# Performance work log

Measured on AMD Instinct MI355X. Metric: run time of the kernel, lower is better.

Reference implementation:

```python
import jax, jax.numpy as jnp
import numpy as np

V, E, HL, HH, T_STEPS, N_STEPS = 32000, 768, 1024, 768, 5, 3
B, S = 8, 256
EPS = 1e-5


def _ln(x, g, b):
    m = jnp.mean(x, axis=-1, keepdims=True)
    v = jnp.var(x, axis=-1, keepdims=True)
    return (x - m) * jax.lax.rsqrt(v + EPS) * g + b


def _gru(x, h, Wi, bi, Wh, bh, lni_g, lni_b, lnh_g, lnh_b):
    # Wi: [3, in_dim, H]; gates stacked in order (r, z, n)
    xi = jnp.einsum('bd,kdh->kbh', x, Wi) + bi[:, None, :]
    hi = jnp.einsum('bh,khg->kbg', h, Wh) + bh[:, None, :]
    xi = _ln(xi, lni_g[:, None, :], lni_b[:, None, :])
    hi = _ln(hi, lnh_g[:, None, :], lnh_b[:, None, :])
    r = jax.nn.sigmoid(xi[0] + hi[0])
    z = jax.nn.sigmoid(xi[1] + hi[1])
    n = jnp.tanh(xi[2] + r * hi[2])
    return (1.0 - z) * n + z * h


def setup_inputs() -> dict:
    key = jax.random.key(0)
    ks = jax.random.split(key, 12)
    lin = E + HH  # low-level cell input dim (x concat h_h)

    def xavier(k, shape, fan_in, fan_out):
        lim = float(np.sqrt(6.0 / (fan_in + fan_out)))
        return jax.random.uniform(k, shape, jnp.float32, -lim, lim)

    inp = {
        'input_ids': jax.random.randint(ks[0], (B, S), 0, V),
        'emb': xavier(ks[1], (V, E), V, E),
        'ln_emb_g': jnp.ones((E,), jnp.float32),
        'ln_emb_b': jnp.zeros((E,), jnp.float32),
        'low_Wi': xavier(ks[2], (3, lin, HL), lin, HL),
        'low_bi': jnp.zeros((3, HL), jnp.float32),
        'low_Wh': xavier(ks[3], (3, HL, HL), HL, HL),
        'low_bh': jnp.zeros((3, HL), jnp.float32),
        'low_lni_g': jnp.ones((3, HL), jnp.float32),
        'low_lni_b': jnp.zeros((3, HL), jnp.float32),
        'low_lnh_g': jnp.ones((3, HL), jnp.float32),
        'low_lnh_b': jnp.zeros((3, HL), jnp.float32),
        'high_Wi': xavier(ks[4], (3, HL, HH), HL, HH),
        'high_bi': jnp.zeros((3, HH), jnp.float32),
        'high_Wh': xavier(ks[5], (3, HH, HH), HH, HH),
        'high_bh': jnp.zeros((3, HH), jnp.float32),
        'high_lni_g': jnp.ones((3, HH), jnp.float32),
        'high_lni_b': jnp.zeros((3, HH), jnp.float32),
        'high_lnh_g': jnp.ones((3, HH), jnp.float32),
        'high_lnh_b': jnp.zeros((3, HH), jnp.float32),
        'Wout': xavier(ks[6], (HH, V), HH, V),
        'bout': jnp.zeros((V,), jnp.float32),
    }
    return inp


def reference(input_ids, emb, ln_emb_g, ln_emb_b,
              low_Wi, low_bi, low_Wh, low_bh,
              low_lni_g, low_lni_b, low_lnh_g, low_lnh_b,
              high_Wi, high_bi, high_Wh, high_bh,
              high_lni_g, high_lni_b, high_lnh_g, high_lnh_b,
              Wout, bout):
    b = input_ids.shape[0]
    h_l0 = jnp.zeros((b, HL), jnp.float32)
    h_h0 = jnp.zeros((b, HH), jnp.float32)

    def step(carry, ids_t):
        h_l, h_h = carry
        x = _ln(emb[ids_t], ln_emb_g, ln_emb_b)  # [B, E]
        for _ in range(N_STEPS):
            for _ in range(T_STEPS):
                h_l = _gru(jnp.concatenate([x, h_h], axis=-1), h_l,
                           low_Wi, low_bi, low_Wh, low_bh,
                           low_lni_g, low_lni_b, low_lnh_g, low_lnh_b)
            h_h = _gru(h_l, h_h,
                       high_Wi, high_bi, high_Wh, high_bh,
                       high_lni_g, high_lni_b, high_lnh_g, high_lnh_b)
        logits_t = h_h @ Wout + bout  # [B, V]
        return (h_l, h_h), logits_t

    _, logits = jax.lax.scan(step, (h_l0, h_h0), input_ids.T)  # [S, B, V]
    return jnp.transpose(logits, (1, 0, 2))  # [B, S, V]
```

## Files before the change

kernel.cpp:

```cpp
#include <hip/hip_runtime.h>
#include <hip/hip_bf16.h>


#define NWG 128
#define NTH 256
#define EPSV 1e-5f

typedef __attribute__((ext_vector_type(4))) float f32x4;
typedef __attribute__((ext_vector_type(8))) short short8;
typedef unsigned long long u64;

struct PArgs {
  const int* ids; const float* emb; const float* lng; const float* lnb;
  const float* lWi; const float* lbi; const float* lWh; const float* lbh;
  const float* llig; const float* llib; const float* llhg; const float* llhb;
  const float* hWi; const float* hbi; const float* hWh; const float* hbh;
  const float* hlig; const float* hlib; const float* hlhg; const float* hlhb;
  int* arr; int* rel; u64* statsG; u64* sredG; float* hlR; float* hhR;
  __hip_bfloat16* hist; float* WiT; float* hWiT; float* hWhT;
};

__device__ __forceinline__ float sigm(float x) { return 1.f / (1.f + __expf(-x)); }
__device__ __forceinline__ float tanh_f(float x) {
  x = fminf(15.f, fmaxf(-15.f, x));
  float e = __expf(2.f * x);
  return (e - 1.f) / (e + 1.f);
}
__device__ __forceinline__ void ast(float* p, float v) {
  __hip_atomic_store(p, v, __ATOMIC_RELAXED, __HIP_MEMORY_SCOPE_AGENT);
}
__device__ __forceinline__ int aldi(const int* p) {
  return __hip_atomic_load(p, __ATOMIC_RELAXED, __HIP_MEMORY_SCOPE_AGENT);
}
__device__ __forceinline__ u64 aldu(const u64* p) {
  return __hip_atomic_load(p, __ATOMIC_RELAXED, __HIP_MEMORY_SCOPE_AGENT);
}
__device__ __forceinline__ void astu(u64* p, u64 v) {
  __hip_atomic_store(p, v, __ATOMIC_RELAXED, __HIP_MEMORY_SCOPE_AGENT);
}
__device__ __forceinline__ void asti(int* p, int v) {
  __hip_atomic_store(p, v, __ATOMIC_RELAXED, __HIP_MEMORY_SCOPE_AGENT);
}
__device__ __forceinline__ void ald4x2(const float* p0, const float* p1,
                                       float4& a, float4& b) {
  asm volatile(
      "global_load_dwordx4 %0, %2, off sc1\n\t"
      "global_load_dwordx4 %1, %3, off sc1\n\t"
      "s_waitcnt vmcnt(0)"
      : "=&v"(a), "=&v"(b)
      : "v"(p0), "v"(p1)
      : "memory");
}
__device__ __forceinline__ void ald4x4(const float* p0, const float* p1,
                                       const float* p2, const float* p3,
                                       float4& a, float4& b, float4& c, float4& d) {
  asm volatile(
      "global_load_dwordx4 %0, %4, off sc1\n\t"
      "global_load_dwordx4 %1, %5, off sc1\n\t"
      "global_load_dwordx4 %2, %6, off sc1\n\t"
      "global_load_dwordx4 %3, %7, off sc1\n\t"
      "s_waitcnt vmcnt(0)"
      : "=&v"(a), "=&v"(b), "=&v"(c), "=&v"(d)
      : "v"(p0), "v"(p1), "v"(p2), "v"(p3)
      : "memory");
}
__device__ __forceinline__ void ald4x8(const float* p0, const float* p1,
                                       const float* p2, const float* p3,
                                       const float* p4, const float* p5,
                                       const float* p6, const float* p7,
                                       float4& a, float4& b, float4& c, float4& d,
                                       float4& e, float4& f, float4& g, float4& h) {
  asm volatile(
      "global_load_dwordx4 %0, %8, off sc1\n\t"
      "global_load_dwordx4 %1, %9, off sc1\n\t"
      "global_load_dwordx4 %2, %10, off sc1\n\t"
      "global_load_dwordx4 %3, %11, off sc1\n\t"
      "global_load_dwordx4 %4, %12, off sc1\n\t"
      "global_load_dwordx4 %5, %13, off sc1\n\t"
      "global_load_dwordx4 %6, %14, off sc1\n\t"
      "global_load_dwordx4 %7, %15, off sc1\n\t"
      "s_waitcnt vmcnt(0)"
      : "=&v"(a), "=&v"(b), "=&v"(c), "=&v"(d),
        "=&v"(e), "=&v"(f), "=&v"(g), "=&v"(h)
      : "v"(p0), "v"(p1), "v"(p2), "v"(p3),
        "v"(p4), "v"(p5), "v"(p6), "v"(p7)
      : "memory");
}

__global__ void __launch_bounds__(NTH) hrm_recur(PArgs P) {
  const int tid = threadIdx.x;

  if (blockIdx.x == NWG) {
    __shared__ float mbuf[192][4];
    __shared__ int mok;
    auto mevent = [&](int e, int lo, int n, float invD, int par) -> bool {
      if (tid < 64) {
        const u64* ap = (const u64*)P.arr + tid;
        int lim = 1 << 22, good = 1;
        for (;;) {
          u64 v = aldu(ap);
          int a0 = (int)(unsigned)(v & 0xffffffffull);
          int a1 = (int)(unsigned)(v >> 32);
          if (__all(a0 >= e && a1 >= e)) break;
          if (--lim == 0) { good = 0; break; }
          __builtin_amdgcn_s_sleep(1);
        }
        if (tid == 0) mok = good;
      }
      __syncthreads();
      bool good = (mok != 0);
      if (good && n > 0) {
        const int rpn = n >> 1;
        const int Q = (n == 48) ? 8 : 16;
        const int wpq = 128 / Q;
        if (tid < rpn * Q) {
          int rp = (lo >> 1) + tid / Q, q = tid % Q;
          const float* b0 = (const float*)(P.statsG + (size_t)par * 128 * 48);
          float4 s; s.x = 0.f; s.y = 0.f; s.z = 0.f; s.w = 0.f;
          #pragma unroll
          for (int blk = 0; blk < 2; ++blk) {
            if (blk == 1 && wpq == 8) break;
            int w0 = q * wpq + blk * 8;
            float4 t0,t1,t2,t3,t4,t5,t6,t7;
            ald4x8(b0 + ((size_t)(w0+0)*48 + rp*2)*2, b0 + ((size_t)(w0+1)*48 + rp*2)*2,
                   b0 + ((size_t)(w0+2)*48 + rp*2)*2, b0 + ((size_t)(w0+3)*48 + rp*2)*2,
                   b0 + ((size_t)(w0+4)*48 + rp*2)*2, b0 + ((size_t)(w0+5)*48 + rp*2)*2,
                   b0 + ((size_t)(w0+6)*48 + rp*2)*2, b0 + ((size_t)(w0+7)*48 + rp*2)*2,
                   t0,t1,t2,t3,t4,t5,t6,t7);
            s.x += t0.x+t1.x+t2.x+t3.x+t4.x+t5.x+t6.x+t7.x;
            s.y += t0.y+t1.y+t2.y+t3.y+t4.y+t5.y+t6.y+t7.y;
            s.z += t0.z+t1.z+t2.z+t3.z+t4.z+t5.z+t6.z+t7.z;
            s.w += t0.w+t1.w+t2.w+t3.w+t4.w+t5.w+t6.w+t7.w;
          }
          mbuf[tid][0] = s.x; mbuf[tid][1] = s.y; mbuf[tid][2] = s.z; mbuf[tid][3] = s.w;
        }
        __syncthreads();
        if (tid < n) {
          int rpl = tid >> 1, comp = tid & 1;
          const int Q2 = (n == 48) ? 8 : 16;
          float s1 = 0.f, s2 = 0.f;
          for (int q = 0; q < Q2; ++q) {
            s1 += mbuf[rpl * Q2 + q][comp * 2 + 0];
            s2 += mbuf[rpl * Q2 + q][comp * 2 + 1];
          }
          float m = s1 * invD;
          float rs = rsqrtf(s2 * invD - m * m + EPSV);
          union { u64 u; float f[2]; } c; c.f[0] = m; c.f[1] = rs;
          astu(P.sredG + (size_t)par * 48 + lo + tid, c.u);
        }
        asm volatile("s_waitcnt vmcnt(0)" ::: "memory");
        __syncthreads();
      }
      int pub = good ? e : (1 << 30);
      if (tid < 8) asti(P.rel + tid * 16, pub);
      return good;
    };

    if (!mevent(1, 0, 0, 0.f, 0)) return;
    int rr = 0;
    #pragma unroll 1
    for (int t = 0; t < 256; ++t) {
      #pragma unroll 1
      for (int nn = 0; nn < 3; ++nn) {
        ++rr;
        if (!mevent(2*rr, 0, 48, 1.f/1024.f, rr & 1)) return;
        if (!mevent(2*rr + 1, 0, 0, 0.f, 0)) return;
        #pragma unroll 1
        for (int it = 1; it < 5; ++it) {
          ++rr;
          if (!mevent(2*rr, 24, 24, 1.f/1024.f, rr & 1)) return;
          if (!mevent(2*rr + 1, 0, 0, 0.f, 0)) return;
        }
        ++rr;
        if (!mevent(2*rr, 0, 48, 1.f/768.f, rr & 1)) return;
        if (!mevent(2*rr + 1, 0, 0, 0.f, 0)) return;
      }
    }
    return;
  }

  __shared__ float WhS[24 * 1024];
  __shared__ float Bb[8 * 1024];
  __shared__ float XW[24 * 8];
  __shared__ float xiNs[24 * 8];
  __shared__ float stg[2][24 * 8];
  __shared__ float sred[96];
  __shared__ float xm[8], xrs[8];
  __shared__ int idsh[8];
  __shared__ int okf;

  const int wg = blockIdx.x;
  const int ks = tid & 31, cg = tid >> 5;
  const int lj8 = wg * 8, lj6 = wg * 6;
  const int rep = wg & 3;

  auto arrive = [&](int e) {
    asm volatile("s_waitcnt vmcnt(0)" ::: "memory");
    __syncthreads();
    if (tid == 0) asti(P.arr + wg, e);
  };
  auto wwait = [&](int e) -> bool {
    if (tid == 0) {
      const int* rp = P.rel + (wg & 7) * 16;
      int lim = 1 << 22, v = 0;
      do {
        v = aldi(rp);
        if (v >= e) break;
        __builtin_amdgcn_s_sleep(1);
      } while (--lim);
      okf = (lim != 0 && v < (1 << 29)) ? 1 : 0;
    }
    __syncthreads();
    return okf != 0;
  };

  auto stage_hl = [&]() {
    const float* base = P.hlR + (size_t)rep * 8192 + tid * 4;
    float4 t0,t1,t2,t3,t4,t5,t6,t7;
    ald4x8(base + 0*1024, base + 1*1024, base + 2*1024, base + 3*1024,
           base + 4*1024, base + 5*1024, base + 6*1024, base + 7*1024,
           t0,t1,t2,t3,t4,t5,t6,t7);
    *(float4*)&Bb[0*1024 + tid*4] = t0; *(float4*)&Bb[1*1024 + tid*4] = t1;
    *(float4*)&Bb[2*1024 + tid*4] = t2; *(float4*)&Bb[3*1024 + tid*4] = t3;
    *(float4*)&Bb[4*1024 + tid*4] = t4; *(float4*)&Bb[5*1024 + tid*4] = t5;
    *(float4*)&Bb[6*1024 + tid*4] = t6; *(float4*)&Bb[7*1024 + tid*4] = t7;
  };
  auto stage_hh = [&]() {
    const float* base = P.hhR + (size_t)rep * 6144;
    int bi[6], ki[6];
    #pragma unroll
    for (int i = 0; i < 6; ++i) {
      int c = i * 256 + tid; int b = c / 192; int k = (c - b * 192) * 4;
      bi[i] = b; ki[i] = k;
    }
    float4 t0,t1,t2,t3,t4,t5;
    ald4x4(base + bi[0]*768 + ki[0], base + bi[1]*768 + ki[1],
           base + bi[2]*768 + ki[2], base + bi[3]*768 + ki[3], t0,t1,t2,t3);
    ald4x2(base + bi[4]*768 + ki[4], base + bi[5]*768 + ki[5], t4,t5);
    *(float4*)&Bb[bi[0]*1024 + ki[0]] = t0; *(float4*)&Bb[bi[1]*1024 + ki[1]] = t1;
    *(float4*)&Bb[bi[2]*1024 + ki[2]] = t2; *(float4*)&Bb[bi[3]*1024 + ki[3]] = t3;
    *(float4*)&Bb[bi[4]*1024 + ki[4]] = t4; *(float4*)&Bb[bi[5]*1024 + ki[5]] = t5;
  };

  auto gemm_lowh = [&](float (&acc)[3][8]) {
    const int c0 = cg * 3;
    const float* w0p = &WhS[(c0 + 0) * 1024];
    const float* w1p = &WhS[(c0 + 1) * 1024];
    const float* w2p = &WhS[(c0 + 2) * 1024];
    #pragma unroll
    for (int i = 0; i < 8; ++i) {
      int k = i * 128 + ks * 4;
      float4 w0 = *(const float4*)&w0p[k];
      float4 w1 = *(const float4*)&w1p[k];
      float4 w2 = *(const float4*)&w2p[k];
      #pragma unroll
      for (int b = 0; b < 8; ++b) {
        float4 h = *(const float4*)&Bb[b * 1024 + k];
        acc[0][b] += w0.x*h.x + w0.y*h.y + w0.z*h.z + w0.w*h.w;
        acc[1][b] += w1.x*h.x + w1.y*h.y + w1.z*h.z + w1.w*h.w;
        acc[2][b] += w2.x*h.x + w2.y*h.y + w2.z*h.z + w2.w*h.w;
      }
    }
  };
  auto gemm_xih = [&](float (&acc)[3][8]) {
    const float* wp[3];
    #pragma unroll
    for (int cc = 0; cc < 3; ++cc) {
      int c = cg * 3 + cc; int g = c >> 3, jj = c & 7;
      wp[cc] = P.WiT + ((size_t)g * 1024 + lj8 + jj) * 1536 + 768;
    }
    #pragma unroll
    for (int i = 0; i < 6; ++i) {
      int k = i * 128 + ks * 4;
      float4 w0 = *(const float4*)&wp[0][k];
      float4 w1 = *(const float4*)&wp[1][k];
      float4 w2 = *(const float4*)&wp[2][k];
      #pragma unroll
      for (int b = 0; b < 8; ++b) {
        float4 h = *(const float4*)&Bb[b * 1024 + k];
        acc[0][b] += w0.x*h.x + w0.y*h.y + w0.z*h.z + w0.w*h.w;
        acc[1][b] += w1.x*h.x + w1.y*h.y + w1.z*h.z + w1.w*h.w;
        acc[2][b] += w2.x*h.x + w2.y*h.y + w2.z*h.z + w2.w*h.w;
      }
    }
  };
  auto gemm_hxi = [&](float (&acc)[3][8]) {
    if (cg >= 6) return;
    const float* wp[3];
    #pragma unroll
    for (int cc = 0; cc < 3; ++cc) {
      int c = cg * 3 + cc; int g = c / 6, jj = c % 6;
      wp[cc] = P.hWiT + ((size_t)g * 768 + lj6 + jj) * 1024;
    }
    #pragma unroll
    for (int i = 0; i < 8; ++i) {
      int k = i * 128 + ks * 4;
      float4 w0 = *(const float4*)&wp[0][k];
      float4 w1 = *(const float4*)&wp[1][k];
      float4 w2 = *(const float4*)&wp[2][k];
      #pragma unroll
      for (int b = 0; b < 8; ++b) {
        float4 h = *(const float4*)&Bb[b * 1024 + k];
        acc[0][b] += w0.x*h.x + w0.y*h.y + w0.z*h.z + w0.w*h.w;
        acc[1][b] += w1.x*h.x + w1.y*h.y + w1.z*h.z + w1.w*h.w;
        acc[2][b] += w2.x*h.x + w2.y*h.y + w2.z*h.z + w2.w*h.w;
      }
    }
  };
  auto gemm_hhh = [&](float (&acc)[3][8]) {
    if (cg >= 6) return;
    const float* wp[3];
    #pragma unroll
    for (int cc = 0; cc < 3; ++cc) {
      int c = cg * 3 + cc; int g = c / 6, jj = c % 6;
      wp[cc] = P.hWhT + ((size_t)g * 768 + lj6 + jj) * 768;
    }
    #pragma unroll
    for (int i = 0; i < 6; ++i) {
      int k = i * 128 + ks * 4;
      float4 w0 = *(const float4*)&wp[0][k];
      float4 w1 = *(const float4*)&wp[1][k];
      float4 w2 = *(const float4*)&wp[2][k];
      #pragma unroll
      for (int b = 0; b < 8; ++b) {
        float4 h = *(const float4*)&Bb[b * 1024 + k];
        acc[0][b] += w0.x*h.x + w0.y*h.y + w0.z*h.z + w0.w*h.w;
        acc[1][b] += w1.x*h.x + w1.y*h.y + w1.z*h.z + w1.w*h.w;
        acc[2][b] += w2.x*h.x + w2.y*h.y + w2.z*h.z + w2.w*h.w;
      }
    }
  };

  auto redstage = [&](float (&acc)[3][8], int set, const float* bias, int dim,
                      int perg, int jb, bool addXW) {
    #pragma unroll
    for (int cc = 0; cc < 3; ++cc)
      #pragma unroll
      for (int b = 0; b < 8; ++b) {
        float v = acc[cc][b];
        #pragma unroll
        for (int m = 1; m < 32; m <<= 1) v += __shfl_xor(v, m, 64);
        acc[cc][b] = v;
      }
    if ((tid & 31) == 0) {
      int cgl = tid >> 5;
      #pragma unroll
      for (int cc = 0; cc < 3; ++cc) {
        int c = cgl * 3 + cc;
        if (c < perg * 3) {
          int g = (perg == 8) ? (c >> 3) : (c / 6);
          int jj = (perg == 8) ? (c & 7) : (c % 6);
          float bs = bias[g * dim + jb + jj];
          #pragma unroll
          for (int b = 0; b < 8; ++b) {
            float v = acc[cc][b] + bs;
            if (addXW) v += XW[c * 8 + b];
            stg[set][c * 8 + b] = v;
          }
        }
      }
    }
  };

  auto stats_put = [&](int par, int set, int perg) {
    if (tid < 24) {
      int g = tid >> 3, b = tid & 7;
      float s1 = 0.f, s2 = 0.f;
      for (int jj = 0; jj < perg; ++jj) {
        float v = stg[set][(g * perg + jj) * 8 + b];
        s1 += v; s2 += v * v;
      }
      union { u64 u; float f[2]; } c; c.f[0] = s1; c.f[1] = s2;
      astu(P.statsG + ((size_t)par * 128 + wg) * 48 + set * 24 + tid, c.u);
    }
  };
  auto sred_read = [&](int par, int lo, int n) {
    if (tid < n) {
      int row = lo + tid;
      union { u64 u; float f[2]; } c;
      c.u = aldu(P.sredG + (size_t)par * 48 + row);
      int set = row / 24, p = row % 24, g = p >> 3, b = p & 7;
      sred[set * 48 + g * 16 + b * 2] = c.f[0];
      sred[set * 48 + g * 16 + b * 2 + 1] = c.f[1];
    }
    __syncthreads();
  };

  auto gate_low = [&](bool isA) {
    if (tid < 64) {
      int jj = tid & 7, b = tid >> 3; int j = lj8 + jj;
      float xin[3], hin[3];
      #pragma unroll
      for (int g = 0; g < 3; ++g) {
        int c = g * 8 + jj;
        if (isA) {
          float m = sred[g * 16 + b * 2], rs = sred[g * 16 + b * 2 + 1];
          float v = (stg[0][c * 8 + b] - m) * rs * P.llig[g * 1024 + j] + P.llib[g * 1024 + j];
          xiNs[c * 8 + b] = v; xin[g] = v;
        } else {
          xin[g] = xiNs[c * 8 + b];
        }
        float m2 = sred[48 + g * 16 + b * 2], rs2 = sred[48 + g * 16 + b * 2 + 1];
        hin[g] = (stg[1][c * 8 + b] - m2) * rs2 * P.llhg[g * 1024 + j] + P.llhb[g * 1024 + j];
      }
      float rg = sigm(xin[0] + hin[0]);
      float zg = sigm(xin[1] + hin[1]);
      float ng = tanh_f(xin[2] + rg * hin[2]);
      float hold = Bb[b * 1024 + j];
      float hv = (1.f - zg) * ng + zg * hold;
      #pragma unroll
      for (int rp = 0; rp < 4; ++rp) ast(&P.hlR[rp * 8192 + b * 1024 + j], hv);
    }
  };

  auto gate_high = [&](int t, int nn) {
    if (tid < 48) {
      int jj = tid % 6, b = tid / 6; int j = lj6 + jj;
      float xin[3], hin[3];
      #pragma unroll
      for (int g = 0; g < 3; ++g) {
        int c = g * 6 + jj;
        float m = sred[g * 16 + b * 2], rs = sred[g * 16 + b * 2 + 1];
        xin[g] = (stg[0][c * 8 + b] - m) * rs * P.hlig[g * 768 + j] + P.hlib[g * 768 + j];
        float m2 = sred[48 + g * 16 + b * 2], rs2 = sred[48 + g * 16 + b * 2 + 1];
        hin[g] = (stg[1][c * 8 + b] - m2) * rs2 * P.hlhg[g * 768 + j] + P.hlhb[g * 768 + j];
      }
      float rg = sigm(xin[0] + hin[0]);
      float zg = sigm(xin[1] + hin[1]);
      float ng = tanh_f(xin[2] + rg * hin[2]);
      float hold = Bb[b * 1024 + j];
      float hv = (1.f - zg) * ng + zg * hold;
      #pragma unroll
      for (int rp = 0; rp < 4; ++rp) ast(&P.hhR[rp * 6144 + b * 768 + j], hv);
      if (nn == 2) P.hist[((size_t)t * 8 + b) * 768 + j] = __float2bfloat16(hv);
    }
  };

  auto xfun = [&](int tt) {
    int b = tid >> 5, u = tid & 31;
    if (tid < 8) idsh[tid] = P.ids[tid * 256 + tt];
    int id = P.ids[b * 256 + tt];
    const float* e = P.emb + (size_t)id * 768;
    float s1 = 0.f, s2 = 0.f;
    #pragma unroll
    for (int q = 0; q < 24; q += 4) {
      float4 v = *(const float4*)&e[u * 24 + q];
      s1 += v.x + v.y + v.z + v.w;
      s2 += v.x*v.x + v.y*v.y + v.z*v.z + v.w*v.w;
    }
    #pragma unroll
    for (int m = 1; m < 32; m <<= 1) { s1 += __shfl_xor(s1, m, 64); s2 += __shfl_xor(s2, m, 64); }
    if (u == 0) { float mm = s1 / 768.f; xm[b] = mm; xrs[b] = rsqrtf(s2 / 768.f - mm * mm + EPSV); }
    __syncthreads();
    float acc[3][8] = {};
    const float* wp[3];
    #pragma unroll
    for (int cc = 0; cc < 3; ++cc) {
      int c = cg * 3 + cc; int g = c >> 3, jj = c & 7;
      wp[cc] = P.WiT + ((size_t)g * 1024 + lj8 + jj) * 1536;
    }
    int idv[8];
    #pragma unroll
    for (int bb = 0; bb < 8; ++bb) idv[bb] = idsh[bb];
    #pragma unroll
    for (int i = 0; i < 6; ++i) {
      int k = i * 128 + ks * 4;
      float4 w0 = *(const float4*)&wp[0][k];
      float4 w1 = *(const float4*)&wp[1][k];
      float4 w2 = *(const float4*)&wp[2][k];
      float4 gam = *(const float4*)&P.lng[k];
      float4 bet = *(const float4*)&P.lnb[k];
      #pragma unroll
      for (int bb = 0; bb < 8; ++bb) {
        float4 xv = *(const float4*)&P.emb[(size_t)idv[bb] * 768 + k];
        float4 xn;
        xn.x = (xv.x - xm[bb]) * xrs[bb] * gam.x + bet.x;
        xn.y = (xv.y - xm[bb]) * xrs[bb] * gam.y + bet.y;
        xn.z = (xv.z - xm[bb]) * xrs[bb] * gam.z + bet.z;
        xn.w = (xv.w - xm[bb]) * xrs[bb] * gam.w + bet.w;
        acc[0][bb] += w0.x*xn.x + w0.y*xn.y + w0.z*xn.z + w0.w*xn.w;
        acc[1][bb] += w1.x*xn.x + w1.y*xn.y + w1.z*xn.z + w1.w*xn.w;
        acc[2][bb] += w2.x*xn.x + w2.y*xn.y + w2.z*xn.z + w2.w*xn.w;
      }
    }
    #pragma unroll
    for (int cc = 0; cc < 3; ++cc)
      #pragma unroll
      for (int bb = 0; bb < 8; ++bb) {
        float v = acc[cc][bb];
        #pragma unroll
        for (int m = 1; m < 32; m <<= 1) v += __shfl_xor(v, m, 64);
        acc[cc][bb] = v;
      }
    if ((tid & 31) == 0) {
      int cgl = tid >> 5;
      #pragma unroll
      for (int cc = 0; cc < 3; ++cc)
        #pragma unroll
        for (int bb = 0; bb < 8; ++bb)
          XW[(cgl * 3 + cc) * 8 + bb] = acc[cc][bb];
    }
    __syncthreads();
  };

  #pragma unroll 1
  for (int g = 0; g < 3; ++g)
    for (int it = 0; it < 6; ++it) {
      int k = it * 256 + tid;
      const float* src = P.lWi + ((size_t)g * 1536 + k) * 1024 + lj8;
      float4 v0 = *(const float4*)src; float4 v1 = *(const float4*)(src + 4);
      float vv[8] = {v0.x, v0.y, v0.z, v0.w, v1.x, v1.y, v1.z, v1.w};
      for (int jj = 0; jj < 8; ++jj)
        P.WiT[((size_t)g * 1024 + lj8 + jj) * 1536 + k] = vv[jj];
    }
  #pragma unroll 1
  for (int g = 0; g < 3; ++g)
    for (int it = 0; it < 4; ++it) {
      int k = it * 256 + tid;
      const float* src = P.hWi + ((size_t)g * 1024 + k) * 768 + lj6;
      float2 a = *(const float2*)src, b2v = *(const float2*)(src + 2), c2v = *(const float2*)(src + 4);
      float vv[6] = {a.x, a.y, b2v.x, b2v.y, c2v.x, c2v.y};
      for (int jj = 0; jj < 6; ++jj)
        P.hWiT[((size_t)g * 768 + lj6 + jj) * 1024 + k] = vv[jj];
    }
  #pragma unroll 1
  for (int g = 0; g < 3; ++g)
    for (int it = 0; it < 3; ++it) {
      int k = it * 256 + tid;
      const float* src = P.hWh + ((size_t)g * 768 + k) * 768 + lj6;
      float2 a = *(const float2*)src, b2v = *(const float2*)(src + 2), c2v = *(const float2*)(src + 4);
      float vv[6] = {a.x, a.y, b2v.x, b2v.y, c2v.x, c2v.y};
      for (int jj = 0; jj < 6; ++jj)
        P.hWhT[((size_t)g * 768 + lj6 + jj) * 768 + k] = vv[jj];
    }
  #pragma unroll 1
  for (int g = 0; g < 3; ++g)
    for (int it = 0; it < 4; ++it) {
      int k = it * 256 + tid;
      const float* src = P.lWh + ((size_t)g * 1024 + k) * 1024 + lj8;
      float4 v0 = *(const float4*)src; float4 v1 = *(const float4*)(src + 4);
      float vv[8] = {v0.x, v0.y, v0.z, v0.w, v1.x, v1.y, v1.z, v1.w};
      for (int jj = 0; jj < 8; ++jj) WhS[(g * 8 + jj) * 1024 + k] = vv[jj];
    }
  __syncthreads();
  xfun(0);
  arrive(1);
  bool alive = wwait(1);

  int rr = 0;
  #pragma unroll 1
  for (int t = 0; alive && t < 256; ++t) {
    #pragma unroll 1
    for (int nn = 0; nn < 3 && alive; ++nn) {
      ++rr; int par = rr & 1;
      {
        stage_hh(); __syncthreads();
        float accX[3][8] = {};
        gemm_xih(accX);
        redstage(accX, 0, P.lbi, 1024, 8, lj8, true);
        __syncthreads();
        stage_hl(); __syncthreads();
        float accH[3][8] = {};
        gemm_lowh(accH);
        redstage(accH, 1, P.lbh, 1024, 8, lj8, false);
        __syncthreads();
        stats_put(par, 0, 8); stats_put(par, 1, 8);
        arrive(2 * rr);
        alive = wwait(2 * rr); if (!alive) break;
        sred_read(par, 0, 48);
        gate_low(true);
        arrive(2 * rr + 1);
        alive = wwait(2 * rr + 1); if (!alive) break;
      }
      #pragma unroll 1
      for (int it = 1; it < 5 && alive; ++it) {
        ++rr; par = rr & 1;
        stage_hl(); __syncthreads();
        float acc2[3][8] = {};
        gemm_lowh(acc2);
        redstage(acc2, 1, P.lbh, 1024, 8, lj8, false);
        __syncthreads();
        stats_put(par, 1, 8);
        arrive(2 * rr);
        alive = wwait(2 * rr); if (!alive) break;
        sred_read(par, 24, 24);
        gate_low(false);
        arrive(2 * rr + 1);
        alive = wwait(2 * rr + 1); if (!alive) break;
      }
      if (!alive) break;
      ++rr; par = rr & 1;
      {
        stage_hl(); __syncthreads();
        float aX[3][8] = {};
        gemm_hxi(aX);
        redstage(aX, 0, P.hbi, 768, 6, lj6, false);
        __syncthreads();
        stage_hh(); __syncthreads();
        float aH[3][8] = {};
        gemm_hhh(aH);
        redstage(aH, 1, P.hbh, 768, 6, lj6, false);
        __syncthreads();
        stats_put(par, 0, 6); stats_put(par, 1, 6);
        arrive(2 * rr);
        alive = wwait(2 * rr); if (!alive) break;
        sred_read(par, 0, 48);
        gate_high(t, nn);
        if (nn == 2 && t < 255) { __syncthreads(); xfun(t + 1); }
        arrive(2 * rr + 1);
        alive = wwait(2 * rr + 1); if (!alive) break;
      }
    }
  }
}

__global__ void __launch_bounds__(256) wout_t(const float* __restrict__ W,
                                              __hip_bfloat16* __restrict__ WT) {
  __shared__ float T[64][65];
  int n0 = blockIdx.x * 64, k0 = blockIdx.y * 64;
  int tid = threadIdx.x;
  int lane16 = tid & 15, grp = tid >> 4;
  #pragma unroll
  for (int i = 0; i < 4; ++i) {
    int kl = i * 16 + grp; int nl = lane16 * 4;
    float4 v = *(const float4*)&W[(size_t)(k0 + kl) * 32000 + n0 + nl];
    T[kl][nl] = v.x; T[kl][nl + 1] = v.y; T[kl][nl + 2] = v.z; T[kl][nl + 3] = v.w;
  }
  __syncthreads();
  #pragma unroll
  for (int i = 0; i < 4; ++i) {
    int nl = i * 16 + grp; int kl = lane16 * 4;
    union { ushort4 v; __hip_bfloat16 h[4]; } u;
    for (int q = 0; q < 4; ++q) u.h[q] = __float2bfloat16(T[kl + q][nl]);
    *(ushort4*)&WT[(size_t)(n0 + nl) * 768 + k0 + kl] = u.v;
  }
}

__global__ void __launch_bounds__(256) logits_gemm(const __hip_bfloat16* __restrict__ Ah,
                                                   const __hip_bfloat16* __restrict__ Bt,
                                                   const float* __restrict__ bias,
                                                   float* __restrict__ out) {
  __shared__ short As[128 * 64];
  __shared__ short Bs[128 * 64];
  int m0 = blockIdx.y * 128, n0 = blockIdx.x * 128;
  int tid = threadIdx.x, lane = tid & 63, w = tid >> 6;
  int wr = w >> 1, wc = w & 1;
  int r16 = lane & 15, khalf = (lane >> 4) * 8;
  f32x4 acc[4][4];
  #pragma unroll
  for (int i = 0; i < 4; ++i)
    #pragma unroll
    for (int j = 0; j < 4; ++j)
      #pragma unroll
      for (int q = 0; q < 4; ++q) acc[i][j][q] = 0.f;

  for (int kt = 0; kt < 12; ++kt) {
    int k0 = kt * 64;
    __syncthreads();
    #pragma unroll
    for (int it = 0; it < 4; ++it) {
      int f = it * 2048 + tid * 8; int row = f >> 6, col = f & 63;
      *(uint4*)&As[f] = *(const uint4*)&Ah[(size_t)(m0 + row) * 768 + k0 + col];
      *(uint4*)&Bs[f] = *(const uint4*)&Bt[(size_t)(n0 + row) * 768 + k0 + col];
    }
    __syncthreads();
    #pragma unroll
    for (int kk = 0; kk < 64; kk += 32) {
      short8 af[4], bfr[4];
      #pragma unroll
      for (int i = 0; i < 4; ++i)
        af[i] = *(short8*)&As[(wr * 64 + i * 16 + r16) * 64 + kk + khalf];
      #pragma unroll
      for (int j = 0; j < 4; ++j)
        bfr[j] = *(short8*)&Bs[(wc * 64 + j * 16 + r16) * 64 + kk + khalf];
      #pragma unroll
      for (int i = 0; i < 4; ++i)
        #pragma unroll
        for (int j = 0; j < 4; ++j)
          acc[i][j] = __builtin_amdgcn_mfma_f32_16x16x32_bf16(af[i], bfr[j], acc[i][j], 0, 0, 0);
    }
  }
  #pragma unroll
  for (int i = 0; i < 4; ++i)
    #pragma unroll
    for (int j = 0; j < 4; ++j)
      #pragma unroll
      for (int q = 0; q < 4; ++q) {
        int m = m0 + wr * 64 + i * 16 + ((lane >> 4) * 4 + q);
        int n = n0 + wc * 64 + j * 16 + (lane & 15);
        out[(size_t)(m & 7) * 8192000 + (size_t)(m >> 3) * 32000 + n] =
            acc[i][j][q] + bias[n];
      }
}

extern "C" void kernel_launch(void* const* d_in, const int* in_sizes, int n_in,
                              void* d_out, int out_size, void* d_ws, size_t ws_size,
                              hipStream_t stream) {
  (void)in_sizes; (void)n_in; (void)out_size; (void)ws_size;
  char* wsb = (char*)d_ws;
  size_t off = 0;
  auto take = [&](size_t bytes) -> void* {
    void* p = wsb + off;
    off += (bytes + 1023) & ~(size_t)1023;
    return p;
  };
  int* arr      = (int*)take((size_t)128 * 4);
  int* rel      = (int*)take((size_t)8 * 16 * 4);
  float* hlR    = (float*)take((size_t)4 * 8 * 1024 * 4);
  float* hhR    = (float*)take((size_t)4 * 8 * 768 * 4);
  size_t state_bytes = off;
  u64* statsG   = (u64*)take((size_t)2 * 128 * 48 * 8);
  u64* sredG    = (u64*)take((size_t)2 * 48 * 8);
  __hip_bfloat16* hist = (__hip_bfloat16*)take((size_t)2048 * 768 * 2);
  float* WiT    = (float*)take((size_t)3 * 1024 * 1536 * 4);
  float* hWiT   = (float*)take((size_t)3 * 768 * 1024 * 4);
  float* hWhT   = (float*)take((size_t)3 * 768 * 768 * 4);
  __hip_bfloat16* WoutT = (__hip_bfloat16*)take((size_t)32000 * 768 * 2);

  hipMemsetAsync(d_ws, 0, state_bytes, stream);

  wout_t<<<dim3(500, 12), 256, 0, stream>>>((const float*)d_in[20], WoutT);

  PArgs A;
  A.ids = (const int*)d_in[0];   A.emb = (const float*)d_in[1];
  A.lng = (const float*)d_in[2]; A.lnb = (const float*)d_in[3];
  A.lWi = (const float*)d_in[4]; A.lbi = (const float*)d_in[5];
  A.lWh = (const float*)d_in[6]; A.lbh = (const float*)d_in[7];
  A.llig = (const float*)d_in[8];  A.llib = (const float*)d_in[9];
  A.llhg = (const float*)d_in[10]; A.llhb = (const float*)d_in[11];
  A.hWi = (const float*)d_in[12];  A.hbi = (const float*)d_in[13];
  A.hWh = (const float*)d_in[14];  A.hbh = (const float*)d_in[15];
  A.hlig = (const float*)d_in[16]; A.hlib = (const float*)d_in[17];
  A.hlhg = (const float*)d_in[18]; A.hlhb = (const float*)d_in[19];
  A.arr = arr; A.rel = rel; A.statsG = statsG; A.sredG = sredG;
  A.hlR = hlR; A.hhR = hhR;
  A.hist = hist; A.WiT = WiT; A.hWiT = hWiT; A.hWhT = hWhT;

  hrm_recur<<<NWG + 1, NTH, 0, stream>>>(A);

  logits_gemm<<<dim3(250, 16), 256, 0, stream>>>(hist, WoutT,
                                                 (const float*)d_in[21],
                                                 (float*)d_out);
}
```

Before: 70.98 ms.

## Replace two-phase master barrier with packed stats release and distributed gate counters

Restructures the persistent kernel's cross-workgroup synchronisation. Before, each round had two master-mediated barriers: stats arrive, then a gate-done barrier. Now the master writes the reduced LayerNorm mean/rstd values together with an epoch word into one release array, and workers poll and read them in the same load. The second barrier becomes a decentralized atomic counter (cntB) that workers check before the next round. The master reduction is also simplified to 4 partial sums per row. This removes one master round-trip and the separate sred read per recurrent step. In exchange it adds counter contention and more complex polling with eight-way counter summation.

```diff
diff --git a/kernel.cpp b/kernel.cpp
--- a/kernel.cpp
+++ b/kernel.cpp
@@ -5,6 +5,7 @@
 #define NWG 128
 #define NTH 256
 #define EPSV 1e-5f
+#define NROUND 4608
 
 typedef __attribute__((ext_vector_type(4))) float f32x4;
 typedef __attribute__((ext_vector_type(8))) short short8;
@@ -16,7 +17,7 @@
   const float* llig; const float* llib; const float* llhg; const float* llhb;
   const float* hWi; const float* hbi; const float* hWh; const float* hbh;
   const float* hlig; const float* hlib; const float* hlhg; const float* hlhb;
-  int* arr; int* rel; u64* statsG; u64* sredG; float* hlR; float* hhR;
+  int* arr; u64* relA; int* cntB; u64* statsG; float* hlR; float* hhR;
   __hip_bfloat16* hist; float* WiT; float* hWiT; float* hWhT;
 };
 
@@ -26,43 +27,23 @@
   float e = __expf(2.f * x);
   return (e - 1.f) / (e + 1.f);
 }
+__device__ __forceinline__ int aldi(const int* p) {
+  return __hip_atomic_load(p, __ATOMIC_RELAXED, __HIP_MEMORY_SCOPE_AGENT);
+}
+__device__ __forceinline__ u64 aldu(const u64* p) {
+  return __hip_atomic_load(p, __ATOMIC_RELAXED, __HIP_MEMORY_SCOPE_AGENT);
+}
+__device__ __forceinline__ void asti(int* p, int v) {
+  __hip_atomic_store(p, v, __ATOMIC_RELAXED, __HIP_MEMORY_SCOPE_AGENT);
+}
+__device__ __forceinline__ u64 pk2(float a, float b) {
+  union { u64 u; float f[2]; } c; c.f[0] = a; c.f[1] = b; return c.u;
+}
+__device__ __forceinline__ void astu(u64* p, u64 v) {
+  __hip_atomic_store(p, v, __ATOMIC_RELAXED, __HIP_MEMORY_SCOPE_AGENT);
+}
 __device__ __forceinline__ void ast(float* p, float v) {
   __hip_atomic_store(p, v, __ATOMIC_RELAXED, __HIP_MEMORY_SCOPE_AGENT);
-}
-__device__ __forceinline__ int aldi(const int* p) {
-  return __hip_atomic_load(p, __ATOMIC_RELAXED, __HIP_MEMORY_SCOPE_AGENT);
-}
-__device__ __forceinline__ u64 aldu(const u64* p) {
-  return __hip_atomic_load(p, __ATOMIC_RELAXED, __HIP_MEMORY_SCOPE_AGENT);
-}
-__device__ __forceinline__ void astu(u64* p, u64 v) {
-  __hip_atomic_store(p, v, __ATOMIC_RELAXED, __HIP_MEMORY_SCOPE_AGENT);
-}
-__device__ __forceinline__ void asti(int* p, int v) {
-  __hip_atomic_store(p, v, __ATOMIC_RELAXED, __HIP_MEMORY_SCOPE_AGENT);
-}
-__device__ __forceinline__ void ald4x2(const float* p0, const float* p1,
-                                       float4& a, float4& b) {
-  asm volatile(
-      "global_load_dwordx4 %0, %2, off sc1\n\t"
-      "global_load_dwordx4 %1, %3, off sc1\n\t"
-      "s_waitcnt vmcnt(0)"
-      : "=&v"(a), "=&v"(b)
-      : "v"(p0), "v"(p1)
-      : "memory");
-}
-__device__ __forceinline__ void ald4x4(const float* p0, const float* p1,
-                                       const float* p2, const float* p3,
-                                       float4& a, float4& b, float4& c, float4& d) {
-  asm volatile(
-      "global_load_dwordx4 %0, %4, off sc1\n\t"
-      "global_load_dwordx4 %1, %5, off sc1\n\t"
-      "global_load_dwordx4 %2, %6, off sc1\n\t"
-      "global_load_dwordx4 %3, %7, off sc1\n\t"
-      "s_waitcnt vmcnt(0)"
-      : "=&v"(a), "=&v"(b), "=&v"(c), "=&v"(d)
-      : "v"(p0), "v"(p1), "v"(p2), "v"(p3)
-      : "memory");
 }
 __device__ __forceinline__ void ald4x8(const float* p0, const float* p1,
                                        const float* p2, const float* p3,
@@ -86,94 +67,92 @@
         "v"(p4), "v"(p5), "v"(p6), "v"(p7)
       : "memory");
 }
+__device__ __forceinline__ void ald4x4(const float* p0, const float* p1,
+                                       const float* p2, const float* p3,
+                                       float4& a, float4& b, float4& c, float4& d) {
+  asm volatile(
+      "global_load_dwordx4 %0, %4, off sc1\n\t"
+      "global_load_dwordx4 %1, %5, off sc1\n\t"
+      "global_load_dwordx4 %2, %6, off sc1\n\t"
+      "global_load_dwordx4 %3, %7, off sc1\n\t"
+      "s_waitcnt vmcnt(0)"
+      : "=&v"(a), "=&v"(b), "=&v"(c), "=&v"(d)
+      : "v"(p0), "v"(p1), "v"(p2), "v"(p3)
+      : "memory");
+}
+__device__ __forceinline__ void ald4x2(const float* p0, const float* p1,
+                                       float4& a, float4& b) {
+  asm volatile(
+      "global_load_dwordx4 %0, %2, off sc1\n\t"
+      "global_load_dwordx4 %1, %3, off sc1\n\t"
+      "s_waitcnt vmcnt(0)"
+      : "=&v"(a), "=&v"(b)
+      : "v"(p0), "v"(p1)
+      : "memory");
+}
 
 __global__ void __launch_bounds__(NTH) hrm_recur(PArgs P) {
   const int tid = threadIdx.x;
 
   if (blockIdx.x == NWG) {
-    __shared__ float mbuf[192][4];
+    __shared__ float mbuf[192][2];
     __shared__ int mok;
-    auto mevent = [&](int e, int lo, int n, float invD, int par) -> bool {
+    #pragma unroll 1
+    for (int r = 1; r <= NROUND; ++r) {
       if (tid < 64) {
         const u64* ap = (const u64*)P.arr + tid;
-        int lim = 1 << 22, good = 1;
+        int lim = 1 << 22, g1 = 1;
         for (;;) {
           u64 v = aldu(ap);
           int a0 = (int)(unsigned)(v & 0xffffffffull);
           int a1 = (int)(unsigned)(v >> 32);
-          if (__all(a0 >= e && a1 >= e)) break;
-          if (--lim == 0) { good = 0; break; }
+          if (__all(a0 >= r && a1 >= r)) break;
+          if (--lim == 0) { g1 = 0; break; }
           __builtin_amdgcn_s_sleep(1);
         }
-        if (tid == 0) mok = good;
+        if (tid == 0) mok = g1;
       }
       __syncthreads();
-      bool good = (mok != 0);
-      if (good && n > 0) {
-        const int rpn = n >> 1;
-        const int Q = (n == 48) ? 8 : 16;
-        const int wpq = 128 / Q;
-        if (tid < rpn * Q) {
-          int rp = (lo >> 1) + tid / Q, q = tid % Q;
-          const float* b0 = (const float*)(P.statsG + (size_t)par * 128 * 48);
-          float4 s; s.x = 0.f; s.y = 0.f; s.z = 0.f; s.w = 0.f;
-          #pragma unroll
-          for (int blk = 0; blk < 2; ++blk) {
-            if (blk == 1 && wpq == 8) break;
-            int w0 = q * wpq + blk * 8;
-            float4 t0,t1,t2,t3,t4,t5,t6,t7;
-            ald4x8(b0 + ((size_t)(w0+0)*48 + rp*2)*2, b0 + ((size_t)(w0+1)*48 + rp*2)*2,
-                   b0 + ((size_t)(w0+2)*48 + rp*2)*2, b0 + ((size_t)(w0+3)*48 + rp*2)*2,
-                   b0 + ((size_t)(w0+4)*48 + rp*2)*2, b0 + ((size_t)(w0+5)*48 + rp*2)*2,
-                   b0 + ((size_t)(w0+6)*48 + rp*2)*2, b0 + ((size_t)(w0+7)*48 + rp*2)*2,
-                   t0,t1,t2,t3,t4,t5,t6,t7);
-            s.x += t0.x+t1.x+t2.x+t3.x+t4.x+t5.x+t6.x+t7.x;
-            s.y += t0.y+t1.y+t2.y+t3.y+t4.y+t5.y+t6.y+t7.y;
-            s.z += t0.z+t1.z+t2.z+t3.z+t4.z+t5.z+t6.z+t7.z;
-            s.w += t0.w+t1.w+t2.w+t3.w+t4.w+t5.w+t6.w+t7.w;
-          }
-          mbuf[tid][0] = s.x; mbuf[tid][1] = s.y; mbuf[tid][2] = s.z; mbuf[tid][3] = s.w;
+      if (!mok) {
+        if (tid < 32)
+          astu(P.relA + (size_t)(tid >> 4) * 64 + (size_t)(tid & 15) * 4,
+               (u64)1 << 30);
+        return;
+      }
+      const int ph = (r - 1) % 6;
+      int lo, n; float invD;
+      if (ph == 0)      { lo = 0;  n = 48; invD = 1.f / 1024.f; }
+      else if (ph == 5) { lo = 0;  n = 48; invD = 1.f / 768.f;  }
+      else              { lo = 24; n = 24; invD = 1.f / 1024.f; }
+      const int par = r & 1;
+      if (tid < n * 4) {
+        int row = lo + (tid >> 2), q = tid & 3;
+        const u64* b0 = P.statsG + (size_t)par * 128 * 48 + (size_t)(q * 32) * 48 + row;
+        float s1 = 0.f, s2 = 0.f;
+        #pragma unroll 8
+        for (int w = 0; w < 32; ++w) {
+          union { u64 u; float f[2]; } c; c.u = aldu(b0 + (size_t)w * 48);
+          s1 += c.f[0]; s2 += c.f[1];
         }
-        __syncthreads();
-        if (tid < n) {
-          int rpl = tid >> 1, comp = tid & 1;
-          const int Q2 = (n == 48) ? 8 : 16;
-          float s1 = 0.f, s2 = 0.f;
-          for (int q = 0; q < Q2; ++q) {
-            s1 += mbuf[rpl * Q2 + q][comp * 2 + 0];
-            s2 += mbuf[rpl * Q2 + q][comp * 2 + 1];
-          }
-          float m = s1 * invD;
-          float rs = rsqrtf(s2 * invD - m * m + EPSV);
-          union { u64 u; float f[2]; } c; c.f[0] = m; c.f[1] = rs;
-          astu(P.sredG + (size_t)par * 48 + lo + tid, c.u);
-        }
-        asm volatile("s_waitcnt vmcnt(0)" ::: "memory");
-        __syncthreads();
-      }
-      int pub = good ? e : (1 << 30);
-      if (tid < 8) asti(P.rel + tid * 16, pub);
-      return good;
-    };
-
-    if (!mevent(1, 0, 0, 0.f, 0)) return;
-    int rr = 0;
-    #pragma unroll 1
-    for (int t = 0; t < 256; ++t) {
-      #pragma unroll 1
-      for (int nn = 0; nn < 3; ++nn) {
-        ++rr;
-        if (!mevent(2*rr, 0, 48, 1.f/1024.f, rr & 1)) return;
-        if (!mevent(2*rr + 1, 0, 0, 0.f, 0)) return;
-        #pragma unroll 1
-        for (int it = 1; it < 5; ++it) {
-          ++rr;
-          if (!mevent(2*rr, 24, 24, 1.f/1024.f, rr & 1)) return;
-          if (!mevent(2*rr + 1, 0, 0, 0.f, 0)) return;
-        }
-        ++rr;
-        if (!mevent(2*rr, 0, 48, 1.f/768.f, rr & 1)) return;
-        if (!mevent(2*rr + 1, 0, 0, 0.f, 0)) return;
+        mbuf[tid][0] = s1; mbuf[tid][1] = s2;
+      }
+      __syncthreads();
+      if (tid < n) {
+        int row = lo + tid;
+        float s1 = mbuf[tid*4][0] + mbuf[tid*4+1][0] + mbuf[tid*4+2][0] + mbuf[tid*4+3][0];
+        float s2 = mbuf[tid*4][1] + mbuf[tid*4+1][1] + mbuf[tid*4+2][1] + mbuf[tid*4+3][1];
+        float m = s1 * invD;
+        float rs = rsqrtf(s2 * invD - m * m + EPSV);
+        astu(P.relA + (size_t)par * 64 + (size_t)(row / 3) * 4 + 1 + row % 3,
+             pk2(m, rs));
+      }
+      asm volatile("s_waitcnt vmcnt(0)" ::: "memory");
+      __syncthreads();
+      {
+        int nhs = (n == 48) ? 16 : 8;
+        int hb  = (n == 48) ? 0 : 8;
+        if (tid < nhs)
+          astu(P.relA + (size_t)par * 64 + (size_t)(hb + tid) * 4, (u64)(unsigned)r);
       }
     }
     return;
@@ -194,24 +173,76 @@
   const int lj8 = wg * 8, lj6 = wg * 6;
   const int rep = wg & 3;
 
-  auto arrive = [&](int e) {
+  auto arriveA = [&](int r) {
     asm volatile("s_waitcnt vmcnt(0)" ::: "memory");
-    __syncthreads();
-    if (tid == 0) asti(P.arr + wg, e);
-  };
-  auto wwait = [&](int e) -> bool {
-    if (tid == 0) {
-      const int* rp = P.rel + (wg & 7) * 16;
-      int lim = 1 << 22, v = 0;
-      do {
-        v = aldi(rp);
-        if (v >= e) break;
+    if (tid == 0) asti(P.arr + wg, r);
+  };
+  auto pollA = [&](int r, bool full) -> bool {
+    if (tid < 64) {
+      int nhs = full ? 16 : 8;
+      bool active = tid < nhs;
+      int hs = full ? tid : (8 + tid);
+      const float* base = (const float*)(P.relA + (size_t)(r & 1) * 64 +
+                                         (size_t)(active ? hs : 0) * 4);
+      int lim = 1 << 22;
+      float4 a = {0,0,0,0}, b = {0,0,0,0};
+      u64 ep = ~0ull;
+      for (;;) {
+        if (active) {
+          ald4x2(base, base + 4, a, b);
+          union { float4 f; u64 u[2]; } ca; ca.f = a; ep = ca.u[0];
+        }
+        bool done = !active || (ep >= (u64)(unsigned)r);
+        if (__all(done)) break;
+        if (--lim == 0) break;
         __builtin_amdgcn_s_sleep(1);
-      } while (--lim);
-      okf = (lim != 0 && v < (1 << 29)) ? 1 : 0;
+      }
+      int bad = (active && ep >= ((u64)1 << 29)) ? 1 : 0;
+      bad = __any(bad) ? 1 : 0;
+      if (active && !bad && lim) {
+        union { float4 f; u64 u[2]; } ca, cb; ca.f = a; cb.f = b;
+        int row0 = hs * 3;
+        #pragma unroll
+        for (int q = 0; q < 3; ++q) {
+          u64 val = (q == 0) ? ca.u[1] : ((q == 1) ? cb.u[0] : cb.u[1]);
+          union { u64 u; float f[2]; } cv; cv.u = val;
+          int row = row0 + q;
+          int set = row / 24, p = row % 24, g = p >> 3, bq = p & 7;
+          sred[set * 48 + g * 16 + bq * 2] = cv.f[0];
+          sred[set * 48 + g * 16 + bq * 2 + 1] = cv.f[1];
+        }
+      }
+      if (tid == 0) okf = (lim != 0 && !bad) ? 1 : 0;
     }
     __syncthreads();
     return okf != 0;
+  };
+  auto waitB = [&](int target) -> bool {
+    if (tid < 64) {
+      bool active = tid < 8;
+      const int* cp = P.cntB + (size_t)(active ? tid : 0) * 32;
+      int lim = 1 << 22;
+      for (;;) {
+        int v = active ? aldi(cp) : 0;
+        int sum = v;
+        sum += __shfl_xor(sum, 1);
+        sum += __shfl_xor(sum, 2);
+        sum += __shfl_xor(sum, 4);
+        int total = __shfl(sum, 0);
+        if (total >= target) break;
+        if (--lim == 0) break;
+        __builtin_amdgcn_s_sleep(2);
+      }
+      if (tid == 0) okf = (lim != 0) ? 1 : 0;
+    }
+    __syncthreads();
+    return okf != 0;
+  };
+  auto gate_commit = [&]() {
+    asm volatile("s_waitcnt vmcnt(0)" ::: "memory");
+    if (tid == 0)
+      __hip_atomic_fetch_add(P.cntB + (size_t)(wg & 7) * 32, 1,
+                             __ATOMIC_RELAXED, __HIP_MEMORY_SCOPE_AGENT);
   };
 
   auto stage_hl = [&]() {
@@ -230,8 +261,8 @@
     int bi[6], ki[6];
     #pragma unroll
     for (int i = 0; i < 6; ++i) {
-      int c = i * 256 + tid; int b = c / 192; int k = (c - b * 192) * 4;
-      bi[i] = b; ki[i] = k;
+      int c = i * 256 + tid; int bq = c / 192; int k = (c - bq * 192) * 4;
+      bi[i] = bq; ki[i] = k;
     }
     float4 t0,t1,t2,t3,t4,t5;
     ald4x4(base + bi[0]*768 + ki[0], base + bi[1]*768 + ki[1],
@@ -254,11 +285,11 @@
       float4 w1 = *(const float4*)&w1p[k];
       float4 w2 = *(const float4*)&w2p[k];
       #pragma unroll
-      for (int b = 0; b < 8; ++b) {
-        float4 h = *(const float4*)&Bb[b * 1024 + k];
-        acc[0][b] += w0.x*h.x + w0.y*h.y + w0.z*h.z + w0.w*h.w;
-        acc[1][b] += w1.x*h.x + w1.y*h.y + w1.z*h.z + w1.w*h.w;
-        acc[2][b] += w2.x*h.x + w2.y*h.y + w2.z*h.z + w2.w*h.w;
+      for (int bq = 0; bq < 8; ++bq) {
+        float4 h = *(const float4*)&Bb[bq * 1024 + k];
+        acc[0][bq] += w0.x*h.x + w0.y*h.y + w0.z*h.z + w0.w*h.w;
+        acc[1][bq] += w1.x*h.x + w1.y*h.y + w1.z*h.z + w1.w*h.w;
+        acc[2][bq] += w2.x*h.x + w2.y*h.y + w2.z*h.z + w2.w*h.w;
       }
     }
   };
@@ -276,11 +307,11 @@
       float4 w1 = *(const float4*)&wp[1][k];
       float4 w2 = *(const float4*)&wp[2][k];
       #pragma unroll
-      for (int b = 0; b < 8; ++b) {
-        float4 h = *(const float4*)&Bb[b * 1024 + k];
-        acc[0][b] += w0.x*h.x + w0.y*h.y + w0.z*h.z + w0.w*h.w;
-        acc[1][b] += w1.x*h.x + w1.y*h.y + w1.z*h.z + w1.w*h.w;
-        acc[2][b] += w2.x*h.x + w2.y*h.y + w2.z*h.z + w2.w*h.w;
+      for (int bq = 0; bq < 8; ++bq) {
+        float4 h = *(const float4*)&Bb[bq * 1024 + k];
+        acc[0][bq] += w0.x*h.x + w0.y*h.y + w0.z*h.z + w0.w*h.w;
+        acc[1][bq] += w1.x*h.x + w1.y*h.y + w1.z*h.z + w1.w*h.w;
+        acc[2][bq] += w2.x*h.x + w2.y*h.y + w2.z*h.z + w2.w*h.w;
       }
     }
   };
@@ -299,11 +330,11 @@
       float4 w1 = *(const float4*)&wp[1][k];
       float4 w2 = *(const float4*)&wp[2][k];
       #pragma unroll
-      for (int b = 0; b < 8; ++b) {
-        float4 h = *(const float4*)&Bb[b * 1024 + k];
-        acc[0][b] += w0.x*h.x + w0.y*h.y + w0.z*h.z + w0.w*h.w;
-        acc[1][b] += w1.x*h.x + w1.y*h.y + w1.z*h.z + w1.w*h.w;
-        acc[2][b] += w2.x*h.x + w2.y*h.y + w2.z*h.z + w2.w*h.w;
+      for (int bq = 0; bq < 8; ++bq) {
+        float4 h = *(const float4*)&Bb[bq * 1024 + k];
+        acc[0][bq] += w0.x*h.x + w0.y*h.y + w0.z*h.z + w0.w*h.w;
+        acc[1][bq] += w1.x*h.x + w1.y*h.y + w1.z*h.z + w1.w*h.w;
+        acc[2][bq] += w2.x*h.x + w2.y*h.y + w2.z*h.z + w2.w*h.w;
       }
     }
   };
@@ -322,11 +353,11 @@
       float4 w1 = *(const float4*)&wp[1][k];
       float4 w2 = *(const float4*)&wp[2][k];
       #pragma unroll
-      for (int b = 0; b < 8; ++b) {
-        float4 h = *(const float4*)&Bb[b * 1024 + k];
-        acc[0][b] += w0.x*h.x + w0.y*h.y + w0.z*h.z + w0.w*h.w;
-        acc[1][b] += w1.x*h.x + w1.y*h.y + w1.z*h.z + w1.w*h.w;
-        acc[2][b] += w2.x*h.x + w2.y*h.y + w2.z*h.z + w2.w*h.w;
+      for (int bq = 0; bq < 8; ++bq) {
+        float4 h = *(const float4*)&Bb[bq * 1024 + k];
+        acc[0][bq] += w0.x*h.x + w0.y*h.y + w0.z*h.z + w0.w*h.w;
+        acc[1][bq] += w1.x*h.x + w1.y*h.y + w1.z*h.z + w1.w*h.w;
+        acc[2][bq] += w2.x*h.x + w2.y*h.y + w2.z*h.z + w2.w*h.w;
       }
     }
   };
@@ -336,11 +367,11 @@
     #pragma unroll
     for (int cc = 0; cc < 3; ++cc)
       #pragma unroll
-      for (int b = 0; b < 8; ++b) {
-        float v = acc[cc][b];
+      for (int bq = 0; bq < 8; ++bq) {
+        float v = acc[cc][bq];
         #pragma unroll
         for (int m = 1; m < 32; m <<= 1) v += __shfl_xor(v, m, 64);
-        acc[cc][b] = v;
+        acc[cc][bq] = v;
       }
     if ((tid & 31) == 0) {
       int cgl = tid >> 5;
@@ -352,10 +383,10 @@
           int jj = (perg == 8) ? (c & 7) : (c % 6);
           float bs = bias[g * dim + jb + jj];
           #pragma unroll
-          for (int b = 0; b < 8; ++b) {
-            float v = acc[cc][b] + bs;
-            if (addXW) v += XW[c * 8 + b];
-            stg[set][c * 8 + b] = v;
+          for (int bq = 0; bq < 8; ++bq) {
+            float v = acc[cc][bq] + bs;
+            if (addXW) v += XW[c * 8 + bq];
+            stg[set][c * 8 + bq] = v;
           }
         }
       }
@@ -370,20 +401,8 @@
         float v = stg[set][(g * perg + jj) * 8 + b];
         s1 += v; s2 += v * v;
       }
-      union { u64 u; float f[2]; } c; c.f[0] = s1; c.f[1] = s2;
-      astu(P.statsG + ((size_t)par * 128 + wg) * 48 + set * 24 + tid, c.u);
-    }
-  };
-  auto sred_read = [&](int par, int lo, int n) {
-    if (tid < n) {
-      int row = lo + tid;
-      union { u64 u; float f[2]; } c;
-      c.u = aldu(P.sredG + (size_t)par * 48 + row);
-      int set = row / 24, p = row % 24, g = p >> 3, b = p & 7;
-      sred[set * 48 + g * 16 + b * 2] = c.f[0];
-      sred[set * 48 + g * 16 + b * 2 + 1] = c.f[1];
-    }
-    __syncthreads();
+      astu(P.statsG + ((size_t)par * 128 + wg) * 48 + set * 24 + tid, pk2(s1, s2));
+    }
   };
 
   auto gate_low = [&](bool isA) {
@@ -437,9 +456,9 @@
   };
 
   auto xfun = [&](int tt) {
-    int b = tid >> 5, u = tid & 31;
+    int bq = tid >> 5, u = tid & 31;
     if (tid < 8) idsh[tid] = P.ids[tid * 256 + tt];
-    int id = P.ids[b * 256 + tt];
+    int id = P.ids[bq * 256 + tt];
     const float* e = P.emb + (size_t)id * 768;
     float s1 = 0.f, s2 = 0.f;
     #pragma unroll
@@ -450,7 +469,7 @@
     }
     #pragma unroll
     for (int m = 1; m < 32; m <<= 1) { s1 += __shfl_xor(s1, m, 64); s2 += __shfl_xor(s2, m, 64); }
-    if (u == 0) { float mm = s1 / 768.f; xm[b] = mm; xrs[b] = rsqrtf(s2 / 768.f - mm * mm + EPSV); }
+    if (u == 0) { float mm = s1 / 768.f; xm[bq] = mm; xrs[bq] = rsqrtf(s2 / 768.f - mm * mm + EPSV); }
     __syncthreads();
     float acc[3][8] = {};
     const float* wp[3];
@@ -544,15 +563,14 @@
     }
   __syncthreads();
   xfun(0);
-  arrive(1);
-  bool alive = wwait(1);
-
-  int rr = 0;
+
+  int r = 1;
+  bool alive = true;
   #pragma unroll 1
-  for (int t = 0; alive && t < 256; ++t) {
+  for (int t = 0; t < 256 && alive; ++t) {
     #pragma unroll 1
     for (int nn = 0; nn < 3 && alive; ++nn) {
-      ++rr; int par = rr & 1;
+      alive = waitB(128 * (r - 1)); if (!alive) break;
       {
         stage_hh(); __syncthreads();
         float accX[3][8] = {};
@@ -564,32 +582,30 @@
         gemm_lowh(accH);
         redstage(accH, 1, P.lbh, 1024, 8, lj8, false);
         __syncthreads();
-        stats_put(par, 0, 8); stats_put(par, 1, 8);
-        arrive(2 * rr);
-        alive = wwait(2 * rr); if (!alive) break;
-        sred_read(par, 0, 48);
+        stats_put(r & 1, 0, 8); stats_put(r & 1, 1, 8);
+        arriveA(r);
+        alive = pollA(r, true); if (!alive) break;
         gate_low(true);
-        arrive(2 * rr + 1);
-        alive = wwait(2 * rr + 1); if (!alive) break;
+        gate_commit();
+        ++r;
       }
       #pragma unroll 1
-      for (int it = 1; it < 5 && alive; ++it) {
-        ++rr; par = rr & 1;
+      for (int it = 1; it < 5; ++it) {
+        alive = waitB(128 * (r - 1)); if (!alive) break;
         stage_hl(); __syncthreads();
         float acc2[3][8] = {};
         gemm_lowh(acc2);
         redstage(acc2, 1, P.lbh, 1024, 8, lj8, false);
         __syncthreads();
-        stats_put(par, 1, 8);
-        arrive(2 * rr);
-        alive = wwait(2 * rr); if (!alive) break;
-        sred_read(par, 24, 24);
+        stats_put(r & 1, 1, 8);
+        arriveA(r);
+        alive = pollA(r, false); if (!alive) break;
         gate_low(false);
-        arrive(2 * rr + 1);
-        alive = wwait(2 * rr + 1); if (!alive) break;
+        gate_commit();
+        ++r;
       }
       if (!alive) break;
-      ++rr; par = rr & 1;
+      alive = waitB(128 * (r - 1)); if (!alive) break;
       {
         stage_hl(); __syncthreads();
         float aX[3][8] = {};
@@ -601,14 +617,13 @@
         gemm_hhh(aH);
         redstage(aH, 1, P.hbh, 768, 6, lj6, false);
         __syncthreads();
-        stats_put(par, 0, 6); stats_put(par, 1, 6);
-        arrive(2 * rr);
-        alive = wwait(2 * rr); if (!alive) break;
-        sred_read(par, 0, 48);
+        stats_put(r & 1, 0, 6); stats_put(r & 1, 1, 6);
+        arriveA(r);
+        alive = pollA(r, true); if (!alive) break;
         gate_high(t, nn);
+        gate_commit();
+        ++r;
         if (nn == 2 && t < 255) { __syncthreads(); xfun(t + 1); }
-        arrive(2 * rr + 1);
-        alive = wwait(2 * rr + 1); if (!alive) break;
       }
     }
   }
@@ -704,17 +719,17 @@
     off += (bytes + 1023) & ~(size_t)1023;
     return p;
   };
-  int* arr      = (int*)take((size_t)128 * 4);
-  int* rel      = (int*)take((size_t)8 * 16 * 4);
-  float* hlR    = (float*)take((size_t)4 * 8 * 1024 * 4);
-  float* hhR    = (float*)take((size_t)4 * 8 * 768 * 4);
+  int* arr    = (int*)take((size_t)128 * 4);
+  u64* relA   = (u64*)take((size_t)2 * 16 * 4 * 8);
+  int* cntB   = (int*)take((size_t)8 * 32 * 4);
+  float* hlR  = (float*)take((size_t)4 * 8 * 1024 * 4);
+  float* hhR  = (float*)take((size_t)4 * 8 * 768 * 4);
   size_t state_bytes = off;
-  u64* statsG   = (u64*)take((size_t)2 * 128 * 48 * 8);
-  u64* sredG    = (u64*)take((size_t)2 * 48 * 8);
+  u64* statsG = (u64*)take((size_t)2 * 128 * 48 * 8);
   __hip_bfloat16* hist = (__hip_bfloat16*)take((size_t)2048 * 768 * 2);
-  float* WiT    = (float*)take((size_t)3 * 1024 * 1536 * 4);
-  float* hWiT   = (float*)take((size_t)3 * 768 * 1024 * 4);
-  float* hWhT   = (float*)take((size_t)3 * 768 * 768 * 4);
+  float* WiT  = (float*)take((size_t)3 * 1024 * 1536 * 4);
+  float* hWiT = (float*)take((size_t)3 * 768 * 1024 * 4);
+  float* hWhT = (float*)take((size_t)3 * 768 * 768 * 4);
   __hip_bfloat16* WoutT = (__hip_bfloat16*)take((size_t)32000 * 768 * 2);
 
   hipMemsetAsync(d_ws, 0, state_bytes, stream);
@@ -732,7 +747,7 @@
   A.hWh = (const float*)d_in[14];  A.hbh = (const float*)d_in[15];
   A.hlig = (const float*)d_in[16]; A.hlib = (const float*)d_in[17];
   A.hlhg = (const float*)d_in[18]; A.hlhb = (const float*)d_in[19];
-  A.arr = arr; A.rel = rel; A.statsG = statsG; A.sredG = sredG;
+  A.arr = arr; A.relA = relA; A.cntB = cntB; A.statsG = statsG;
   A.hlR = hlR; A.hhR = hhR;
   A.hist = hist; A.WiT = WiT; A.hWiT = hWiT; A.hWhT = hWhT;
 
```

Result: slower. 83.55 ms (+17.7%).
